# Optimization experiments

Hardware: AMD Instinct MI355X
Metric: run time of the kernel (lower is better)

Reference implementation:

```python
import jax, jax.numpy as jnp
import numpy as np
import math

B, S, D = 4, 2048, 768
H = 12
DH = D // H  # 64
NEG = -1e10

def setup_inputs() -> dict:
    key = jax.random.key(0)
    ks = jax.random.split(key, 8)
    scale = 0.02
    return {
        "hidden_states": jax.random.normal(ks[0], (B, S, D), dtype=jnp.float32),
        "attention_mask": jnp.zeros((B, 1, 1, S), dtype=jnp.float32),
        "Wq": jax.random.normal(ks[1], (D, D), dtype=jnp.float32) * scale,
        "bq": jnp.zeros((D,), dtype=jnp.float32),
        "Wk": jax.random.normal(ks[2], (D, D), dtype=jnp.float32) * scale,
        "bk": jnp.zeros((D,), dtype=jnp.float32),
        "Wv": jax.random.normal(ks[3], (D, D), dtype=jnp.float32) * scale,
        "bv": jnp.zeros((D,), dtype=jnp.float32),
    }

def reference(hidden_states, attention_mask, Wq, bq, Wk, bk, Wv, bv):
    # Linear projections; note attention_mask is accepted but unused, matching the torch module.
    def split_heads(x):  # [B,S,D] -> [B,H,S,DH]
        return x.reshape(B, S, H, DH).transpose(0, 2, 1, 3)
    q = split_heads(hidden_states @ Wq + bq)
    k = split_heads(hidden_states @ Wk + bk)
    v = split_heads(hidden_states @ Wv + bv)
    scores = jnp.einsum("bhqd,bhkd->bhqk", q, k) / math.sqrt(DH)
    causal = jnp.tril(jnp.ones((S, S), dtype=bool))  # masked_fill(mask==0, -1e10)
    scores = jnp.where(causal, scores, NEG)
    probs = jax.nn.softmax(scores, axis=-1)
    # dropout prob = 0.0 (eval) -> identity
    ctx = jnp.einsum("bhqk,bhkd->bhqd", probs, v)
    return ctx.transpose(0, 2, 1, 3).reshape(B, S, D)
```

## Files before the change

### kernel.cpp

```cpp
#include <hip/hip_runtime.h>
#include <hip/hip_bf16.h>

#define B_  4
#define S_  2048
#define D_  768
#define H_  12
#define DH_ 64

typedef __bf16 bf16;
typedef __attribute__((ext_vector_type(8))) __bf16 bf16x8;
typedef __attribute__((ext_vector_type(4))) __bf16 bf16x4;
typedef __attribute__((ext_vector_type(4))) float floatx4;

__device__ __forceinline__ int chunk_off2(int qt2) {
    if (qt2 < 4)  return qt2;
    if (qt2 < 8)  return 4 + 2 * (qt2 - 4);
    if (qt2 < 12) return 12 + 3 * (qt2 - 8);
    return 24 + 4 * (qt2 - 12);
}

__device__ __forceinline__ unsigned pack_bf16(float a, float b) {
    unsigned short ua = __builtin_bit_cast(unsigned short, (bf16)a);
    unsigned short ub = __builtin_bit_cast(unsigned short, (bf16)b);
    return (unsigned)ua | ((unsigned)ub << 16);
}

__global__ __launch_bounds__(256) void cvt_f32_bf16(const float* __restrict__ in,
                                                    bf16* __restrict__ out, int n4) {
    int i = blockIdx.x * 256 + threadIdx.x;
    if (i < n4) {
        float4 v = ((const float4*)in)[i];
        bf16x4 o;
        o[0] = (bf16)v.x; o[1] = (bf16)v.y; o[2] = (bf16)v.z; o[3] = (bf16)v.w;
        *(bf16x4*)(out + (size_t)i * 4) = o;
    }
}

__global__ __launch_bounds__(256) void w_transpose(const float* __restrict__ w0,
                                                   const float* __restrict__ w1,
                                                   const float* __restrict__ w2,
                                                   bf16* __restrict__ Wt)
{
    const int which = blockIdx.z;
    const float* W = (which == 0) ? w0 : (which == 1 ? w1 : w2);
    bf16* dst = Wt + (size_t)which * D_ * D_;
    __shared__ bf16 t[64 * 72];
    const int k0 = blockIdx.x * 64, n0 = blockIdx.y * 64;
    const int tid = threadIdx.x;
    {
        int r = tid >> 2;
        int c0 = (tid & 3) * 16;
        #pragma unroll
        for (int q = 0; q < 4; q++) {
            float4 v = *(const float4*)(W + (size_t)(k0 + r) * D_ + n0 + c0 + q * 4);
            t[(c0 + q * 4 + 0) * 72 + r] = (bf16)v.x;
            t[(c0 + q * 4 + 1) * 72 + r] = (bf16)v.y;
            t[(c0 + q * 4 + 2) * 72 + r] = (bf16)v.z;
            t[(c0 + q * 4 + 3) * 72 + r] = (bf16)v.w;
        }
    }
    __syncthreads();
    {
        int n = tid >> 3, seg = tid & 7;
        *(bf16x8*)(dst + (size_t)(n0 + n) * D_ + k0 + seg * 8) =
            *(const bf16x8*)(t + n * 72 + seg * 8);
        *(bf16x8*)(dst + (size_t)(n0 + n + 32) * D_ + k0 + seg * 8) =
            *(const bf16x8*)(t + (n + 32) * 72 + seg * 8);
    }
}

__global__ __launch_bounds__(256) void qkv_gemm(
    const bf16* __restrict__ Xb, const bf16* __restrict__ Wt,
    const float* __restrict__ bq, const float* __restrict__ bk,
    const float* __restrict__ bv, bf16* __restrict__ QKV)
{
    const int which = blockIdx.z;
    const bf16* Wm = Wt + (size_t)which * D_ * D_;
    const float* bias = (which == 0) ? bq : (which == 1 ? bk : bv);
    bf16* out = QKV + (size_t)which * B_ * H_ * S_ * DH_;

    __shared__ bf16 As[128 * 72];
    __shared__ bf16 Bs[128 * 72];

    const int tid  = threadIdx.x;
    const int wave = tid >> 6, lane = tid & 63;
    const int wr = wave >> 1, wc = wave & 1;
    const int g = lane >> 4, ln = lane & 15;
    const int m0 = blockIdx.x * 128, n0 = blockIdx.y * 128;

    floatx4 acc[4][4];
    #pragma unroll
    for (int i = 0; i < 4; i++)
        #pragma unroll
        for (int j = 0; j < 4; j++)
            acc[i][j] = (floatx4){0.f, 0.f, 0.f, 0.f};

    int row_[4], seg_[4];
    #pragma unroll
    for (int t = 0; t < 4; t++) { int fc = tid + t * 256; row_[t] = fc >> 3; seg_[t] = fc & 7; }

    bf16x8 apf[4], bpf[4];
    #pragma unroll
    for (int t = 0; t < 4; t++) {
        apf[t] = *(const bf16x8*)(Xb + (size_t)(m0 + row_[t]) * D_ + seg_[t] * 8);
        bpf[t] = *(const bf16x8*)(Wm + (size_t)(n0 + row_[t]) * D_ + seg_[t] * 8);
    }

    for (int k0 = 0; k0 < D_; k0 += 64) {
        __syncthreads();
        #pragma unroll
        for (int t = 0; t < 4; t++) {
            *(bf16x8*)(As + row_[t] * 72 + seg_[t] * 8) = apf[t];
            *(bf16x8*)(Bs + row_[t] * 72 + seg_[t] * 8) = bpf[t];
        }
        __syncthreads();
        if (k0 + 64 < D_) {
            #pragma unroll
            for (int t = 0; t < 4; t++) {
                apf[t] = *(const bf16x8*)(Xb + (size_t)(m0 + row_[t]) * D_ + k0 + 64 + seg_[t] * 8);
                bpf[t] = *(const bf16x8*)(Wm + (size_t)(n0 + row_[t]) * D_ + k0 + 64 + seg_[t] * 8);
            }
        }
        #pragma unroll
        for (int ks = 0; ks < 2; ks++) {
            bf16x8 af[4], bfr[4];
            #pragma unroll
            for (int i = 0; i < 4; i++)
                af[i] = *(const bf16x8*)(As + (wr * 64 + i * 16 + ln) * 72 + ks * 32 + g * 8);
            #pragma unroll
            for (int j = 0; j < 4; j++)
                bfr[j] = *(const bf16x8*)(Bs + (wc * 64 + j * 16 + ln) * 72 + ks * 32 + g * 8);
            #pragma unroll
            for (int i = 0; i < 4; i++)
                #pragma unroll
                for (int j = 0; j < 4; j++)
                    acc[i][j] = __builtin_amdgcn_mfma_f32_16x16x32_bf16(af[i], bfr[j], acc[i][j], 0, 0, 0);
        }
    }

    const float sc = (which == 0) ? 0.125f : 1.0f;
    #pragma unroll
    for (int i = 0; i < 4; i++) {
        #pragma unroll
        for (int j = 0; j < 4; j++) {
            int col = n0 + wc * 64 + j * 16 + ln;
            float bv_ = bias[col];
            int h = col >> 6, dh = col & 63;
            int rowbase = m0 + wr * 64 + i * 16 + g * 4;
            int b = rowbase >> 11, s0 = rowbase & 2047;
            if (which == 2) {
                bf16x4 o;
                #pragma unroll
                for (int r = 0; r < 4; r++) o[r] = (bf16)(acc[i][j][r] + bv_);
                *(bf16x4*)(out + ((size_t)((b * H_ + h) * DH_ + dh)) * S_ + s0) = o;
            } else {
                #pragma unroll
                for (int r = 0; r < 4; r++)
                    out[(((size_t)(b * H_ + h) * S_ + s0 + r) << 6) + dh] =
                        (bf16)((acc[i][j][r] + bv_) * sc);
            }
        }
    }
}

__global__ __launch_bounds__(256) void attn_chunk(const bf16* __restrict__ QKV,
                                                  float* __restrict__ out,
                                                  bf16* __restrict__ Opart,
                                                  float* __restrict__ Lpart)
{
    const int cid = 39 - blockIdx.x;
    const int bh = blockIdx.y;
    const int b = bh / H_, h = bh % H_;

    int qt2, c;
    if (cid < 4)       { qt2 = cid; c = 0; }
    else if (cid < 12) { int t = cid - 4;  qt2 = 4 + (t >> 1);  c = t & 1; }
    else if (cid < 24) { int t = cid - 12; qt2 = 8 + t / 3;     c = t - 3 * (t / 3); }
    else               { int t = cid - 24; qt2 = 12 + (t >> 2); c = t & 3; }
    const int nch = (2 * qt2 + 9) >> 3;
    const int kt0 = c * 8;
    const int kt1 = min(kt0 + 7, 2 * qt2 + 1);

    const size_t MAT = (size_t)B_ * H_ * S_ * DH_;
    const bf16* Q  = QKV +           (size_t)bh * S_ * DH_;
    const bf16* K  = QKV + MAT +     (size_t)bh * S_ * DH_;
    const bf16* Vt = QKV + 2 * MAT + (size_t)bh * S_ * DH_;

    __shared__ bf16 Ks[64 * 72];
    __shared__ bf16 Vts[64 * 72];

    const int tid  = threadIdx.x;
    const int wave = tid >> 6, lane = tid & 63;
    const int g = lane >> 4, ln = lane & 15;
    const int srow = tid >> 3, sseg = tid & 7;
    const int qbase = qt2 * 128;

    bf16x8 qf[2][2];
    #pragma unroll
    for (int t = 0; t < 2; t++) {
        const bf16* qrow = Q + (size_t)(qbase + t * 64 + wave * 16 + ln) * DH_;
        qf[t][0] = *(const bf16x8*)(qrow + g * 8);
        qf[t][1] = *(const bf16x8*)(qrow + 32 + g * 8);
    }

    bf16x8 ones;
    #pragma unroll
    for (int i = 0; i < 8; i++) ones[i] = (bf16)1.0f;

    floatx4 accO[2][4];
    #pragma unroll
    for (int t = 0; t < 2; t++)
        #pragma unroll
        for (int j = 0; j < 4; j++) accO[t][j] = (floatx4){0.f, 0.f, 0.f, 0.f};
    floatx4 accL[2] = {(floatx4){0.f, 0.f, 0.f, 0.f}, (floatx4){0.f, 0.f, 0.f, 0.f}};

    const bf16* kptr = K  + (size_t)(kt0 * 64 + srow) * DH_ + sseg * 8;
    const bf16* vptr = Vt + (size_t)srow * S_ + kt0 * 64 + sseg * 8;
    bf16x8 ka = *(const bf16x8*)kptr;
    bf16x8 kb = *(const bf16x8*)(kptr + 32 * DH_);
    bf16x8 va = *(const bf16x8*)vptr;
    bf16x8 vb = *(const bf16x8*)(vptr + (size_t)32 * S_);

    const int s0lane = ((lane >> 4) & 1) * 32 + ln;
    const bool hi = (lane >= 32);

    for (int kt = kt0; kt <= kt1; ++kt) {
        __syncthreads();
        *(bf16x8*)(Ks  + srow * 72 + sseg * 8) = ka;
        *(bf16x8*)(Ks  + (srow + 32) * 72 + sseg * 8) = kb;
        *(bf16x8*)(Vts + srow * 72 + sseg * 8) = va;
        *(bf16x8*)(Vts + (srow + 32) * 72 + sseg * 8) = vb;
        __syncthreads();
        if (kt < kt1) {
            kptr += 64 * DH_;
            vptr += 64;
            ka = *(const bf16x8*)kptr;
            kb = *(const bf16x8*)(kptr + 32 * DH_);
            va = *(const bf16x8*)vptr;
            vb = *(const bf16x8*)(vptr + (size_t)32 * S_);
        }

        bf16x8 kf[4][2];
        #pragma unroll
        for (int j = 0; j < 4; j++)
            #pragma unroll
            for (int cc = 0; cc < 2; cc++)
                kf[j][cc] = *(const bf16x8*)(Ks + (j * 16 + ln) * 72 + cc * 32 + g * 8);

        floatx4 accS[2][4];
        #pragma unroll
        for (int t = 0; t < 2; t++)
            #pragma unroll
            for (int j = 0; j < 4; j++) accS[t][j] = (floatx4){0.f, 0.f, 0.f, 0.f};
        #pragma unroll
        for (int t = 0; t < 2; t++)
            #pragma unroll
            for (int j = 0; j < 4; j++)
                #pragma unroll
                for (int cc = 0; cc < 2; cc++)
                    accS[t][j] = __builtin_amdgcn_mfma_f32_16x16x32_bf16(
                        kf[j][cc], qf[t][cc], accS[t][j], 0, 0, 0);

        unsigned pd0[2][4], pd1[2][4];
        #pragma unroll
        for (int t = 0; t < 2; t++) {
            const int qg = qbase + t * 64 + wave * 16 + ln;
            const bool domask = (kt >= 2 * qt2 + t);
            #pragma unroll
            for (int j = 0; j < 4; j++) {
                float p[4];
                #pragma unroll
                for (int r = 0; r < 4; r++) {
                    p[r] = __expf(accS[t][j][r]);
                    if (domask) {
                        int key = kt * 64 + j * 16 + g * 4 + r;
                        if (key > qg) p[r] = 0.f;
                    }
                }
                pd0[t][j] = pack_bf16(p[0], p[1]);
                pd1[t][j] = pack_bf16(p[2], p[3]);
            }
        }

        #pragma unroll
        for (int cc = 0; cc < 2; cc++) {
            bf16x8 ptf[2];
            #pragma unroll
            for (int t = 0; t < 2; t++) {
                unsigned a0 = __shfl(pd0[t][2 * cc],     s0lane);
                unsigned b0 = __shfl(pd0[t][2 * cc + 1], s0lane);
                unsigned a1 = __shfl(pd1[t][2 * cc],     s0lane);
                unsigned b1 = __shfl(pd1[t][2 * cc + 1], s0lane);
                unsigned a2 = __shfl(pd0[t][2 * cc],     s0lane + 16);
                unsigned b2 = __shfl(pd0[t][2 * cc + 1], s0lane + 16);
                unsigned a3 = __shfl(pd1[t][2 * cc],     s0lane + 16);
                unsigned b3 = __shfl(pd1[t][2 * cc + 1], s0lane + 16);
                uint4 w;
                w.x = hi ? b0 : a0;
                w.y = hi ? b1 : a1;
                w.z = hi ? b2 : a2;
                w.w = hi ? b3 : a3;
                ptf[t] = __builtin_bit_cast(bf16x8, w);
                accL[t] = __builtin_amdgcn_mfma_f32_16x16x32_bf16(ones, ptf[t], accL[t], 0, 0, 0);
            }
            #pragma unroll
            for (int j = 0; j < 4; j++) {
                bf16x8 vf = *(const bf16x8*)(Vts + (j * 16 + ln) * 72 + cc * 32 + g * 8);
                #pragma unroll
                for (int t = 0; t < 2; t++)
                    accO[t][j] = __builtin_amdgcn_mfma_f32_16x16x32_bf16(
                        vf, ptf[t], accO[t][j], 0, 0, 0);
            }
        }
    }

    if (nch == 1) {
        #pragma unroll
        for (int t = 0; t < 2; t++) {
            float inv = 1.0f / accL[t][0];
            int q = qbase + t * 64 + wave * 16 + ln;
            float* orow = out + (size_t)(b * S_ + q) * D_ + h * DH_;
            #pragma unroll
            for (int j = 0; j < 4; j++) {
                float4 o;
                o.x = accO[t][j][0] * inv; o.y = accO[t][j][1] * inv;
                o.z = accO[t][j][2] * inv; o.w = accO[t][j][3] * inv;
                *(float4*)(orow + j * 16 + g * 4) = o;
            }
        }
    } else {
        const int chunk = bh * 40 + chunk_off2(qt2) + c;
        bf16* obase = Opart + (size_t)chunk * 8192;
        #pragma unroll
        for (int t = 0; t < 2; t++) {
            int ql = t * 64 + wave * 16 + ln;
            #pragma unroll
            for (int j = 0; j < 4; j++) {
                bf16x4 o;
                #pragma unroll
                for (int r = 0; r < 4; r++) o[r] = (bf16)accO[t][j][r];
                *(bf16x4*)(obase + ql * 64 + j * 16 + g * 4) = o;
            }
            if (g == 0) Lpart[chunk * 128 + ql] = accL[t][0];
        }
    }
}

__global__ __launch_bounds__(256) void attn_reduce(const bf16* __restrict__ Opart,
                                                   const float* __restrict__ Lpart,
                                                   float* __restrict__ out)
{
    const int qt2 = 4 + blockIdx.x;
    const int bh = blockIdx.y;
    const int b = bh / H_, h = bh % H_;
    const int nch = (2 * qt2 + 9) >> 3;
    const int cb = bh * 40 + chunk_off2(qt2);

    const int e = threadIdx.x;
    const int ql = e >> 1, dh0 = (e & 1) * 32;

    float o[32];
    #pragma unroll
    for (int i = 0; i < 32; i++) o[i] = 0.f;
    float l = 0.f;

    for (int cidx = 0; cidx < nch; cidx++) {
        const bf16* p = Opart + (size_t)(cb + cidx) * 8192 + ql * 64 + dh0;
        #pragma unroll
        for (int m = 0; m < 4; m++) {
            bf16x8 v = *(const bf16x8*)(p + m * 8);
            #pragma unroll
            for (int k = 0; k < 8; k++) o[m * 8 + k] += (float)v[k];
        }
        l += Lpart[(cb + cidx) * 128 + ql];
    }
    float inv = 1.0f / l;
    float* orow = out + (size_t)(b * S_ + qt2 * 128 + ql) * D_ + h * DH_ + dh0;
    #pragma unroll
    for (int m = 0; m < 8; m++) {
        float4 v;
        v.x = o[m * 4 + 0] * inv; v.y = o[m * 4 + 1] * inv;
        v.z = o[m * 4 + 2] * inv; v.w = o[m * 4 + 3] * inv;
        *(float4*)(orow + m * 4) = v;
    }
}

extern "C" void kernel_launch(void* const* d_in, const int* in_sizes, int n_in,
                              void* d_out, int out_size, void* d_ws, size_t ws_size,
                              hipStream_t stream) {
    const float* hs = (const float*)d_in[0];
    const float* Wq = (const float*)d_in[2];
    const float* bq = (const float*)d_in[3];
    const float* Wk = (const float*)d_in[4];
    const float* bk = (const float*)d_in[5];
    const float* Wv = (const float*)d_in[6];
    const float* bv = (const float*)d_in[7];
    float* out = (float*)d_out;

    bf16* Xb    = (bf16*)d_ws;
    bf16* Wt    = Xb + (size_t)8192 * 768;
    bf16* QKV   = Wt + (size_t)3 * 768 * 768;
    bf16* Opart = QKV + (size_t)3 * B_ * H_ * S_ * DH_;
    float* Lpart = (float*)(Opart + (size_t)1920 * 8192);

    cvt_f32_bf16<<<6144, 256, 0, stream>>>(hs, Xb, 1572864);
    w_transpose<<<dim3(12, 12, 3), 256, 0, stream>>>(Wq, Wk, Wv, Wt);
    qkv_gemm<<<dim3(64, 6, 3), 256, 0, stream>>>(Xb, Wt, bq, bk, bv, QKV);
    attn_chunk<<<dim3(40, 48), 256, 0, stream>>>(QKV, out, Opart, Lpart);
    attn_reduce<<<dim3(12, 48), 256, 0, stream>>>(Opart, Lpart, out);
}
```

Before: 210.5 us.

## Switch attention inner loop to 32x32x16 MFMA with per-lane row sums

Rewrites the attention kernel's inner loop to use 32x32x16 bf16 MFMA tiles, with each wave owning 32 query rows instead of two 16-row tiles. The P-matrix transpose now needs a single xor-32 shuffle exchange instead of eight indexed shuffles per step. The softmax denominator is accumulated in scalar registers rather than through an extra MFMA against a ones vector. This is meant to cut LDS reads of K, shuffle traffic and MFMA issue count. The trade-off is different register pressure and a different accumulator layout at the output stores.

```diff
diff --git a/kernel.cpp b/kernel.cpp
--- a/kernel.cpp
+++ b/kernel.cpp
@@ -11,6 +11,7 @@
 typedef __attribute__((ext_vector_type(8))) __bf16 bf16x8;
 typedef __attribute__((ext_vector_type(4))) __bf16 bf16x4;
 typedef __attribute__((ext_vector_type(4))) float floatx4;
+typedef __attribute__((ext_vector_type(16))) float floatx16;
 
 __device__ __forceinline__ int chunk_off2(int qt2) {
     if (qt2 < 4)  return qt2;
@@ -191,28 +192,25 @@
 
     const int tid  = threadIdx.x;
     const int wave = tid >> 6, lane = tid & 63;
-    const int g = lane >> 4, ln = lane & 15;
+    const int l31 = lane & 31, lh = lane >> 5;
     const int srow = tid >> 3, sseg = tid & 7;
     const int qbase = qt2 * 128;
-
-    bf16x8 qf[2][2];
-    #pragma unroll
-    for (int t = 0; t < 2; t++) {
-        const bf16* qrow = Q + (size_t)(qbase + t * 64 + wave * 16 + ln) * DH_;
-        qf[t][0] = *(const bf16x8*)(qrow + g * 8);
-        qf[t][1] = *(const bf16x8*)(qrow + 32 + g * 8);
-    }
-
-    bf16x8 ones;
-    #pragma unroll
-    for (int i = 0; i < 8; i++) ones[i] = (bf16)1.0f;
-
-    floatx4 accO[2][4];
-    #pragma unroll
-    for (int t = 0; t < 2; t++)
-        #pragma unroll
-        for (int j = 0; j < 4; j++) accO[t][j] = (floatx4){0.f, 0.f, 0.f, 0.f};
-    floatx4 accL[2] = {(floatx4){0.f, 0.f, 0.f, 0.f}, (floatx4){0.f, 0.f, 0.f, 0.f}};
+    const int qs = qbase + wave * 32;
+    const int q = qs + l31;
+
+    bf16x8 qf[4];
+    {
+        const bf16* qrow = Q + (size_t)q * DH_ + lh * 8;
+        #pragma unroll
+        for (int s = 0; s < 4; s++) qf[s] = *(const bf16x8*)(qrow + s * 16);
+    }
+
+    floatx16 accO[2];
+    #pragma unroll
+    for (int dt = 0; dt < 2; dt++)
+        #pragma unroll
+        for (int e = 0; e < 16; e++) accO[dt][e] = 0.f;
+    float Lrun = 0.f;
 
     const bf16* kptr = K  + (size_t)(kt0 * 64 + srow) * DH_ + sseg * 8;
     const bf16* vptr = Vt + (size_t)srow * S_ + kt0 * 64 + sseg * 8;
@@ -220,9 +218,6 @@
     bf16x8 kb = *(const bf16x8*)(kptr + 32 * DH_);
     bf16x8 va = *(const bf16x8*)vptr;
     bf16x8 vb = *(const bf16x8*)(vptr + (size_t)32 * S_);
-
-    const int s0lane = ((lane >> 4) & 1) * 32 + ln;
-    const bool hi = (lane >= 32);
 
     for (int kt = kt0; kt <= kt1; ++kt) {
         __syncthreads();
@@ -240,109 +235,86 @@
             vb = *(const bf16x8*)(vptr + (size_t)32 * S_);
         }
 
-        bf16x8 kf[4][2];
-        #pragma unroll
-        for (int j = 0; j < 4; j++)
-            #pragma unroll
-            for (int cc = 0; cc < 2; cc++)
-                kf[j][cc] = *(const bf16x8*)(Ks + (j * 16 + ln) * 72 + cc * 32 + g * 8);
-
-        floatx4 accS[2][4];
-        #pragma unroll
-        for (int t = 0; t < 2; t++)
-            #pragma unroll
-            for (int j = 0; j < 4; j++) accS[t][j] = (floatx4){0.f, 0.f, 0.f, 0.f};
-        #pragma unroll
-        for (int t = 0; t < 2; t++)
-            #pragma unroll
-            for (int j = 0; j < 4; j++)
-                #pragma unroll
-                for (int cc = 0; cc < 2; cc++)
-                    accS[t][j] = __builtin_amdgcn_mfma_f32_16x16x32_bf16(
-                        kf[j][cc], qf[t][cc], accS[t][j], 0, 0, 0);
-
-        unsigned pd0[2][4], pd1[2][4];
-        #pragma unroll
-        for (int t = 0; t < 2; t++) {
-            const int qg = qbase + t * 64 + wave * 16 + ln;
-            const bool domask = (kt >= 2 * qt2 + t);
-            #pragma unroll
-            for (int j = 0; j < 4; j++) {
+        floatx16 accS[2];
+        #pragma unroll
+        for (int kk = 0; kk < 2; kk++) {
+            #pragma unroll
+            for (int e = 0; e < 16; e++) accS[kk][e] = 0.f;
+            #pragma unroll
+            for (int s = 0; s < 4; s++) {
+                bf16x8 kf = *(const bf16x8*)(Ks + (kk * 32 + l31) * 72 + s * 16 + lh * 8);
+                accS[kk] = __builtin_amdgcn_mfma_f32_32x32x16_bf16(kf, qf[s], accS[kk], 0, 0, 0);
+            }
+        }
+
+        unsigned pk1[2][4], pk2[2][4];
+        const bool domask = (kt * 64 + 63 > qs);
+        #pragma unroll
+        for (int kk = 0; kk < 2; kk++) {
+            const int keyb = kt * 64 + kk * 32 + 4 * lh;
+            #pragma unroll
+            for (int rq = 0; rq < 4; rq++) {
                 float p[4];
                 #pragma unroll
-                for (int r = 0; r < 4; r++) {
-                    p[r] = __expf(accS[t][j][r]);
-                    if (domask) {
-                        int key = kt * 64 + j * 16 + g * 4 + r;
-                        if (key > qg) p[r] = 0.f;
-                    }
+                for (int rr = 0; rr < 4; rr++) {
+                    float v = __expf(accS[kk][4 * rq + rr]);
+                    if (domask && (keyb + 8 * rq + rr > q)) v = 0.f;
+                    p[rr] = v;
+                    Lrun += v;
                 }
-                pd0[t][j] = pack_bf16(p[0], p[1]);
-                pd1[t][j] = pack_bf16(p[2], p[3]);
-            }
-        }
-
-        #pragma unroll
-        for (int cc = 0; cc < 2; cc++) {
-            bf16x8 ptf[2];
-            #pragma unroll
-            for (int t = 0; t < 2; t++) {
-                unsigned a0 = __shfl(pd0[t][2 * cc],     s0lane);
-                unsigned b0 = __shfl(pd0[t][2 * cc + 1], s0lane);
-                unsigned a1 = __shfl(pd1[t][2 * cc],     s0lane);
-                unsigned b1 = __shfl(pd1[t][2 * cc + 1], s0lane);
-                unsigned a2 = __shfl(pd0[t][2 * cc],     s0lane + 16);
-                unsigned b2 = __shfl(pd0[t][2 * cc + 1], s0lane + 16);
-                unsigned a3 = __shfl(pd1[t][2 * cc],     s0lane + 16);
-                unsigned b3 = __shfl(pd1[t][2 * cc + 1], s0lane + 16);
-                uint4 w;
-                w.x = hi ? b0 : a0;
-                w.y = hi ? b1 : a1;
-                w.z = hi ? b2 : a2;
-                w.w = hi ? b3 : a3;
-                ptf[t] = __builtin_bit_cast(bf16x8, w);
-                accL[t] = __builtin_amdgcn_mfma_f32_16x16x32_bf16(ones, ptf[t], accL[t], 0, 0, 0);
-            }
-            #pragma unroll
-            for (int j = 0; j < 4; j++) {
-                bf16x8 vf = *(const bf16x8*)(Vts + (j * 16 + ln) * 72 + cc * 32 + g * 8);
-                #pragma unroll
-                for (int t = 0; t < 2; t++)
-                    accO[t][j] = __builtin_amdgcn_mfma_f32_16x16x32_bf16(
-                        vf, ptf[t], accO[t][j], 0, 0, 0);
-            }
-        }
-    }
+                pk1[kk][rq] = pack_bf16(p[0], p[1]);
+                pk2[kk][rq] = pack_bf16(p[2], p[3]);
+            }
+        }
+
+        #pragma unroll
+        for (int s = 0; s < 4; s++) {
+            const int kk = s >> 1, sl = s & 1;
+            unsigned sendA = lh ? pk1[kk][2 * sl] : pk1[kk][2 * sl + 1];
+            unsigned sendB = lh ? pk2[kk][2 * sl] : pk2[kk][2 * sl + 1];
+            unsigned recvA = __shfl_xor(sendA, 32, 64);
+            unsigned recvB = __shfl_xor(sendB, 32, 64);
+            uint4 w;
+            w.x = lh ? recvA : pk1[kk][2 * sl];
+            w.y = lh ? recvB : pk2[kk][2 * sl];
+            w.z = lh ? pk1[kk][2 * sl + 1] : recvA;
+            w.w = lh ? pk2[kk][2 * sl + 1] : recvB;
+            bf16x8 ptf = __builtin_bit_cast(bf16x8, w);
+            #pragma unroll
+            for (int dt = 0; dt < 2; dt++) {
+                bf16x8 vf = *(const bf16x8*)(Vts + (dt * 32 + l31) * 72 + s * 16 + lh * 8);
+                accO[dt] = __builtin_amdgcn_mfma_f32_32x32x16_bf16(vf, ptf, accO[dt], 0, 0, 0);
+            }
+        }
+    }
+
+    const float L = Lrun + __shfl_xor(Lrun, 32, 64);
 
     if (nch == 1) {
-        #pragma unroll
-        for (int t = 0; t < 2; t++) {
-            float inv = 1.0f / accL[t][0];
-            int q = qbase + t * 64 + wave * 16 + ln;
-            float* orow = out + (size_t)(b * S_ + q) * D_ + h * DH_;
-            #pragma unroll
-            for (int j = 0; j < 4; j++) {
+        const float inv = 1.0f / L;
+        float* orow = out + (size_t)(b * S_ + q) * D_ + h * DH_;
+        #pragma unroll
+        for (int dt = 0; dt < 2; dt++)
+            #pragma unroll
+            for (int rq = 0; rq < 4; rq++) {
                 float4 o;
-                o.x = accO[t][j][0] * inv; o.y = accO[t][j][1] * inv;
-                o.z = accO[t][j][2] * inv; o.w = accO[t][j][3] * inv;
-                *(float4*)(orow + j * 16 + g * 4) = o;
-            }
-        }
+                o.x = accO[dt][4 * rq + 0] * inv; o.y = accO[dt][4 * rq + 1] * inv;
+                o.z = accO[dt][4 * rq + 2] * inv; o.w = accO[dt][4 * rq + 3] * inv;
+                *(float4*)(orow + dt * 32 + 8 * rq + 4 * lh) = o;
+            }
     } else {
         const int chunk = bh * 40 + chunk_off2(qt2) + c;
-        bf16* obase = Opart + (size_t)chunk * 8192;
-        #pragma unroll
-        for (int t = 0; t < 2; t++) {
-            int ql = t * 64 + wave * 16 + ln;
-            #pragma unroll
-            for (int j = 0; j < 4; j++) {
+        bf16* obase = Opart + (size_t)chunk * 8192 + (wave * 32 + l31) * 64;
+        #pragma unroll
+        for (int dt = 0; dt < 2; dt++)
+            #pragma unroll
+            for (int rq = 0; rq < 4; rq++) {
                 bf16x4 o;
                 #pragma unroll
-                for (int r = 0; r < 4; r++) o[r] = (bf16)accO[t][j][r];
-                *(bf16x4*)(obase + ql * 64 + j * 16 + g * 4) = o;
-            }
-            if (g == 0) Lpart[chunk * 128 + ql] = accL[t][0];
-        }
+                for (int rr = 0; rr < 4; rr++) o[rr] = (bf16)accO[dt][4 * rq + rr];
+                *(bf16x4*)(obase + dt * 32 + 8 * rq + 4 * lh) = o;
+            }
+        if (lh == 0) Lpart[chunk * 128 + wave * 32 + l31] = L;
     }
 }
 
```

New measurement: 207.0 us. About the same (-1.7%).
